# Kernel optimization log

Hardware: AMD Instinct MI355X
Metric: run time of the kernel (lower is better)

The kernel has to match this reference:

```python
import jax, jax.numpy as jnp
import numpy as np

B, T, C, NH = 8, 1024, 768, 12

def setup_inputs() -> dict:
    key = jax.random.key(0)
    k1, k2, k3 = jax.random.split(key, 3)
    x = jax.random.normal(k1, (B, T, C), dtype=jnp.float32)
    Wqkv = jax.random.normal(k2, (C, 3 * C), dtype=jnp.float32) * 0.02
    bqkv = jnp.zeros((3 * C,), dtype=jnp.float32)
    Wproj = jax.random.normal(k3, (C, C), dtype=jnp.float32) * 0.02
    bproj = jnp.zeros((C,), dtype=jnp.float32)
    return {"x": x, "Wqkv": Wqkv, "bqkv": bqkv, "Wproj": Wproj, "bproj": bproj}

def reference(x, Wqkv, bqkv, Wproj, bproj):
    b, t, c = x.shape
    hs = c // NH
    qkv = x @ Wqkv + bqkv  # [B,T,3C]
    q, k, v = jnp.split(qkv, 3, axis=2)
    # [B,T,C] -> [B,NH,T,hs]
    q = q.reshape(b, t, NH, hs).transpose(0, 2, 1, 3)
    k = k.reshape(b, t, NH, hs).transpose(0, 2, 1, 3)
    v = v.reshape(b, t, NH, hs).transpose(0, 2, 1, 3)
    att = jnp.einsum('bhqd,bhkd->bhqk', q, k) * (hs ** -0.5)
    causal = jnp.tril(jnp.ones((t, t), dtype=bool))
    att = jnp.where(causal[None, None], att, jnp.finfo(att.dtype).min)
    att = jax.nn.softmax(att, axis=-1)
    y = jnp.einsum('bhqk,bhkd->bhqd', att, v)
    y = y.transpose(0, 2, 1, 3).reshape(b, t, c)
    return y @ Wproj + bproj
```

## Files before the change

### kernel.cpp

```cpp
#include <hip/hip_runtime.h>

constexpr int Bb  = 8;
constexpr int Tt  = 1024;
constexpr int Cc  = 768;
constexpr int NHh = 12;
constexpr int HS  = 64;
constexpr int C3  = 3 * Cc;

typedef short bf16x8 __attribute__((ext_vector_type(8)));
typedef float f32x4  __attribute__((ext_vector_type(4)));

__device__ inline short bf16r(float f) {
    unsigned u = __float_as_uint(f);
    u += 0x7FFF + ((u >> 16) & 1);
    return (short)(u >> 16);
}
__device__ inline short bf16h(float f) {
    return (short)((__float_as_uint(f) + 0x8000u) >> 16);
}

__global__ __launch_bounds__(256)
void f32_to_bf16(const float* __restrict__ in, short* __restrict__ out, int n) {
    int i = (blockIdx.x * 256 + threadIdx.x) * 4;
    if (i < n) {
        float4 v = *(const float4*)(in + i);
        short4 o;
        o.x = bf16r(v.x); o.y = bf16r(v.y); o.z = bf16r(v.z); o.w = bf16r(v.w);
        *(short4*)(out + i) = o;
    }
}

__global__ __launch_bounds__(1024)
void transpose_to_bf16(const float* __restrict__ in, short* __restrict__ out,
                       int R, int C) {
    __shared__ short tile[32][33];
    int c = blockIdx.x * 32 + threadIdx.x;
    int r = blockIdx.y * 32 + threadIdx.y;
    tile[threadIdx.y][threadIdx.x] = bf16r(in[(size_t)r * C + c]);
    __syncthreads();
    int oc   = blockIdx.y * 32 + threadIdx.x;
    int orow = blockIdx.x * 32 + threadIdx.y;
    out[(size_t)orow * R + oc] = tile[threadIdx.x][threadIdx.y];
}

__global__ __launch_bounds__(256)
void transpose_v(const short* __restrict__ qkv, short* __restrict__ vt) {
    __shared__ short tile[64][65];
    const int bh = blockIdx.y;
    const int b = bh / NHh, h = bh % NHh;
    const int t0 = blockIdx.x * 64;
    const int tx = threadIdx.x & 63, ty = threadIdx.x >> 6;
    const short* src = qkv + ((size_t)b * Tt + t0) * C3 + 2 * Cc + h * HS;
#pragma unroll
    for (int r = 0; r < 16; ++r)
        tile[ty * 16 + r][tx] = src[(size_t)(ty * 16 + r) * C3 + tx];
    __syncthreads();
    short* dst = vt + (size_t)bh * HS * Tt + t0;
#pragma unroll
    for (int r = 0; r < 16; ++r)
        dst[(size_t)(ty * 16 + r) * Tt + tx] = tile[tx][ty * 16 + r];
}

template <int MI, int OB>
__global__ __launch_bounds__(256)
void gemm_mfma_bias(const short* __restrict__ A, const short* __restrict__ Bt,
                    const float* __restrict__ bias, void* __restrict__ Cout,
                    int M, int N, int K) {
    constexpr int TM = MI * 32;
    __shared__ short Als[TM * 64];
    __shared__ short Bls[128 * 64];

    const int t = threadIdx.x, w = t >> 6, lane = t & 63;
    const int m0 = blockIdx.y * TM, n0 = blockIdx.x * 128;

    const int sr = t >> 3;
    const int sg = ((t & 7) ^ (sr & 7)) * 8;

    const short* Ag[MI];
#pragma unroll
    for (int q = 0; q < MI; ++q)
        Ag[q] = A + (size_t)(m0 + q * 32 + sr) * K + sg;
    const short* Bg[4];
#pragma unroll
    for (int q = 0; q < 4; ++q)
        Bg[q] = Bt + (size_t)(n0 + q * 32 + sr) * K + sg;

    char* AlsB = (char*)Als + w * 1024;
    char* BlsB = (char*)Bls + w * 1024;

    const int wm = (w >> 1) * (MI * 16), wn = (w & 1) * 64;
    const int laneM = lane & 15, laneG = lane >> 4;

    f32x4 acc[MI][4] = {};

    for (int kt = 0; kt < K; kt += 64) {
        __syncthreads();
#pragma unroll
        for (int q = 0; q < MI; ++q)
            __builtin_amdgcn_global_load_lds(
                (const __attribute__((address_space(1))) void*)(Ag[q] + kt),
                (__attribute__((address_space(3))) void*)(AlsB + q * 4096), 16, 0, 0);
#pragma unroll
        for (int q = 0; q < 4; ++q)
            __builtin_amdgcn_global_load_lds(
                (const __attribute__((address_space(1))) void*)(Bg[q] + kt),
                (__attribute__((address_space(3))) void*)(BlsB + q * 4096), 16, 0, 0);
        __syncthreads();

#pragma unroll
        for (int ks = 0; ks < 2; ++ks) {
            const int kx = (((ks << 2) + laneG) ^ (laneM & 7)) * 8;
            bf16x8 af[MI], bfr[4];
#pragma unroll
            for (int i = 0; i < MI; ++i)
                af[i] = *(const bf16x8*)&Als[(wm + i * 16 + laneM) * 64 + kx];
#pragma unroll
            for (int j = 0; j < 4; ++j)
                bfr[j] = *(const bf16x8*)&Bls[(wn + j * 16 + laneM) * 64 + kx];
#pragma unroll
            for (int i = 0; i < MI; ++i)
#pragma unroll
                for (int j = 0; j < 4; ++j)
                    acc[i][j] = __builtin_amdgcn_mfma_f32_16x16x32_bf16(
                        af[i], bfr[j], acc[i][j], 0, 0, 0);
        }
    }

    const int rowBase = m0 + wm + laneG * 4;
    const int colBase = n0 + wn + laneM;
#pragma unroll
    for (int j = 0; j < 4; ++j) {
        const int col = colBase + j * 16;
        const float bv = bias[col];
#pragma unroll
        for (int i = 0; i < MI; ++i) {
#pragma unroll
            for (int r = 0; r < 4; ++r) {
                const int row = rowBase + i * 16 + r;
                const float v = acc[i][j][r] + bv;
                if (OB) ((short*)Cout)[(size_t)row * N + col] = bf16r(v);
                else    ((float*)Cout)[(size_t)row * N + col] = v;
            }
        }
    }
}

__global__ __launch_bounds__(256)
void flash_attn(const short* __restrict__ qkv, const short* __restrict__ vt,
                short* __restrict__ y) {
    const int bh = blockIdx.x % (Bb * NHh);
    const int pi = blockIdx.x / (Bb * NHh);
    const int h  = bh % NHh, b = bh / NHh;
    const int t = threadIdx.x, w = t >> 6, lane = t & 63;
    const int laneM = lane & 15, laneG = lane >> 4;

    __shared__ short Kls[64 * 64];
    __shared__ short Vls[64 * 64];
    __shared__ short Pls[4][16 * 72];

    const size_t bT = (size_t)b * Tt;

    bf16x8 onesb;
#pragma unroll
    for (int j = 0; j < 8; ++j) onesb[j] = (short)0x3F80;

    const int srow = t >> 3;
    const int gpos = t & 7;
    char* KlsB = (char*)Kls + w * 1024;
    char* VlsB = (char*)Vls + w * 1024;
    const int gs0 = (gpos ^ (srow & 7)) * 8;

    const short* Kbase = qkv + (bT + srow) * C3 + Cc + h * HS + gs0;
    const short* Vbase = vt + ((size_t)bh * HS + srow) * Tt + gs0;

    constexpr float cexp = 0.18033688f;
    constexpr float moff = -5.7707801f;

#pragma unroll 1
    for (int sub = 0; sub < 2; ++sub) {
        const int qt = sub ? (15 - pi) : pi;
        const int q0 = qt * 64;

        const short* qp = qkv + (bT + q0 + w * 16 + laneM) * C3 + h * HS;
        const bf16x8 qf0 = *(const bf16x8*)(qp + laneG * 8);
        const bf16x8 qf1 = *(const bf16x8*)(qp + 32 + laneG * 8);

        f32x4 oacc[4] = {};
        f32x4 lacc   = {};

        const short* Kg = Kbase;
        const short* Vg = Vbase;
#pragma unroll 1
        for (int kt = 0; kt <= qt; ++kt, Kg += 64 * C3, Vg += 64) {
            __syncthreads();
            __builtin_amdgcn_global_load_lds(
                (const __attribute__((address_space(1))) void*)Kg,
                (__attribute__((address_space(3))) void*)(KlsB), 16, 0, 0);
            __builtin_amdgcn_global_load_lds(
                (const __attribute__((address_space(1))) void*)(Kg + 32 * C3),
                (__attribute__((address_space(3))) void*)(KlsB + 4096), 16, 0, 0);
            __builtin_amdgcn_global_load_lds(
                (const __attribute__((address_space(1))) void*)Vg,
                (__attribute__((address_space(3))) void*)(VlsB), 16, 0, 0);
            __builtin_amdgcn_global_load_lds(
                (const __attribute__((address_space(1))) void*)(Vg + 32 * Tt),
                (__attribute__((address_space(3))) void*)(VlsB + 4096), 16, 0, 0);
            __syncthreads();

            f32x4 sacc[4] = {};
#pragma unroll
            for (int ks = 0; ks < 2; ++ks) {
                const bf16x8 qf = ks ? qf1 : qf0;
#pragma unroll
                for (int nb = 0; nb < 4; ++nb) {
                    const int key = nb * 16 + laneM;
                    const bf16x8 kf = *(const bf16x8*)
                        &Kls[key * 64 + (((ks << 2) + laneG) ^ (key & 7)) * 8];
                    sacc[nb] = __builtin_amdgcn_mfma_f32_16x16x32_bf16(
                        qf, kf, sacc[nb], 0, 0, 0);
                }
            }

            if (kt == qt) {
#pragma unroll
                for (int nb = 0; nb < 4; ++nb) {
                    const int col = nb * 16 + laneM;
#pragma unroll
                    for (int r = 0; r < 4; ++r) {
                        const int row = w * 16 + laneG * 4 + r;
                        if (col > row) sacc[nb][r] = -1e30f;
                    }
                }
            }

            short* Pw = &Pls[w][0];
#pragma unroll
            for (int r = 0; r < 4; ++r)
#pragma unroll
                for (int nb = 0; nb < 4; ++nb) {
                    const float pv = exp2f(fmaf(sacc[nb][r], cexp, moff));
                    Pw[(laneG * 4 + r) * 72 + nb * 16 + laneM] = bf16h(pv);
                }

#pragma unroll
            for (int ks = 0; ks < 2; ++ks) {
                const bf16x8 pf = *(const bf16x8*)&Pw[laneM * 72 + ks * 32 + laneG * 8];
                lacc = __builtin_amdgcn_mfma_f32_16x16x32_bf16(pf, onesb, lacc, 0, 0, 0);
#pragma unroll
                for (int nb = 0; nb < 4; ++nb) {
                    const int d = nb * 16 + laneM;
                    const bf16x8 vf = *(const bf16x8*)
                        &Vls[d * 64 + (((ks << 2) + laneG) ^ (d & 7)) * 8];
                    oacc[nb] = __builtin_amdgcn_mfma_f32_16x16x32_bf16(
                        pf, vf, oacc[nb], 0, 0, 0);
                }
            }
        }

        short* yp = y + (bT + q0 + w * 16) * Cc + h * HS;
#pragma unroll
        for (int r = 0; r < 4; ++r) {
            const float inv = 1.f / lacc[r];
#pragma unroll
            for (int nb = 0; nb < 4; ++nb)
                yp[(size_t)(laneG * 4 + r) * Cc + nb * 16 + laneM] = bf16r(oacc[nb][r] * inv);
        }
    }
}

extern "C" void kernel_launch(void* const* d_in, const int* in_sizes, int n_in,
                              void* d_out, int out_size, void* d_ws, size_t ws_size,
                              hipStream_t stream) {
    const float* x     = (const float*)d_in[0];
    const float* Wqkv  = (const float*)d_in[1];
    const float* bqkv  = (const float*)d_in[2];
    const float* Wproj = (const float*)d_in[3];
    const float* bproj = (const float*)d_in[4];

    constexpr int M = Bb * Tt;
    short* xb     = (short*)d_ws;
    short* wqkvT  = xb     + (size_t)M * Cc;
    short* wprojT = wqkvT  + (size_t)C3 * Cc;
    short* qkv    = wprojT + (size_t)Cc * Cc;
    short* yatt   = qkv    + (size_t)M * C3;
    short* vt     = yatt   + (size_t)M * Cc;

    f32_to_bf16<<<dim3((M * Cc) / 1024), dim3(256), 0, stream>>>(x, xb, M * Cc);
    transpose_to_bf16<<<dim3(C3 / 32, Cc / 32), dim3(32, 32), 0, stream>>>(Wqkv, wqkvT, Cc, C3);
    transpose_to_bf16<<<dim3(Cc / 32, Cc / 32), dim3(32, 32), 0, stream>>>(Wproj, wprojT, Cc, Cc);

    gemm_mfma_bias<4, 1><<<dim3(C3 / 128, M / 128), dim3(256), 0, stream>>>(
        xb, wqkvT, bqkv, qkv, M, C3, Cc);

    transpose_v<<<dim3(Tt / 64, Bb * NHh), dim3(256), 0, stream>>>(qkv, vt);

    flash_attn<<<dim3(Bb * NHh * 8), dim3(256), 0, stream>>>(qkv, vt, yatt);

    gemm_mfma_bias<2, 0><<<dim3(Cc / 128, M / 64), dim3(256), 0, stream>>>(
        yatt, wprojT, bproj, (float*)d_out, M, Cc, Cc);
}
```

Baseline: 199.2 us.

## Double-buffer GEMM LDS tiles with K-step 32 and prefetch next tile

Restructures the bf16 MFMA GEMM main loop to use two LDS buffers of K-width 32 instead of one buffer of width 64. The next K-slice is issued via global_load_lds into the alternate buffer right after the current fragments are read, which leaves one barrier per iteration instead of two. The goal is to overlap global-to-LDS traffic with MFMA work. The trade-offs are twice as many loop iterations, each with half the MFMA work per barrier, and a new swizzle pattern that could raise LDS bank conflicts. The new layout also requires MI to be even.

```diff
diff --git a/kernel.cpp b/kernel.cpp
--- a/kernel.cpp
+++ b/kernel.cpp
@@ -67,63 +67,78 @@
                     const float* __restrict__ bias, void* __restrict__ Cout,
                     int M, int N, int K) {
     constexpr int TM = MI * 32;
-    __shared__ short Als[TM * 64];
-    __shared__ short Bls[128 * 64];
+    __shared__ __align__(16) short Als[2][TM * 32];
+    __shared__ __align__(16) short Bls[2][128 * 32];
 
     const int t = threadIdx.x, w = t >> 6, lane = t & 63;
     const int m0 = blockIdx.y * TM, n0 = blockIdx.x * 128;
 
-    const int sr = t >> 3;
-    const int sg = ((t & 7) ^ (sr & 7)) * 8;
-
-    const short* Ag[MI];
-#pragma unroll
-    for (int q = 0; q < MI; ++q)
-        Ag[q] = A + (size_t)(m0 + q * 32 + sr) * K + sg;
-    const short* Bg[4];
-#pragma unroll
-    for (int q = 0; q < 4; ++q)
-        Bg[q] = Bt + (size_t)(n0 + q * 32 + sr) * K + sg;
-
-    char* AlsB = (char*)Als + w * 1024;
-    char* BlsB = (char*)Bls + w * 1024;
+    const int sr = t >> 2;
+    const int lg = ((t & 3) ^ ((t >> 3) & 3)) * 8;
+
+    const short* Ag[MI / 2];
+#pragma unroll
+    for (int q = 0; q < MI / 2; ++q)
+        Ag[q] = A + (size_t)(m0 + q * 64 + sr) * K + lg;
+    const short* Bg[2];
+#pragma unroll
+    for (int q = 0; q < 2; ++q)
+        Bg[q] = Bt + (size_t)(n0 + q * 64 + sr) * K + lg;
+
+    const int wq = w * 1024;
 
     const int wm = (w >> 1) * (MI * 16), wn = (w & 1) * 64;
     const int laneM = lane & 15, laneG = lane >> 4;
+    const int kx = (laneG ^ ((laneM >> 1) & 3)) * 8;
 
     f32x4 acc[MI][4] = {};
 
-    for (int kt = 0; kt < K; kt += 64) {
+    const int nk = K / 32;
+
+#pragma unroll
+    for (int q = 0; q < MI / 2; ++q)
+        __builtin_amdgcn_global_load_lds(
+            (const __attribute__((address_space(1))) void*)(Ag[q]),
+            (__attribute__((address_space(3))) void*)((char*)&Als[0][0] + q * 4096 + wq), 16, 0, 0);
+#pragma unroll
+    for (int q = 0; q < 2; ++q)
+        __builtin_amdgcn_global_load_lds(
+            (const __attribute__((address_space(1))) void*)(Bg[q]),
+            (__attribute__((address_space(3))) void*)((char*)&Bls[0][0] + q * 4096 + wq), 16, 0, 0);
+
+    for (int kt = 0; kt < nk; ++kt) {
         __syncthreads();
-#pragma unroll
-        for (int q = 0; q < MI; ++q)
-            __builtin_amdgcn_global_load_lds(
-                (const __attribute__((address_space(1))) void*)(Ag[q] + kt),
-                (__attribute__((address_space(3))) void*)(AlsB + q * 4096), 16, 0, 0);
-#pragma unroll
-        for (int q = 0; q < 4; ++q)
-            __builtin_amdgcn_global_load_lds(
-                (const __attribute__((address_space(1))) void*)(Bg[q] + kt),
-                (__attribute__((address_space(3))) void*)(BlsB + q * 4096), 16, 0, 0);
-        __syncthreads();
-
-#pragma unroll
-        for (int ks = 0; ks < 2; ++ks) {
-            const int kx = (((ks << 2) + laneG) ^ (laneM & 7)) * 8;
-            bf16x8 af[MI], bfr[4];
-#pragma unroll
-            for (int i = 0; i < MI; ++i)
-                af[i] = *(const bf16x8*)&Als[(wm + i * 16 + laneM) * 64 + kx];
+
+        const short* Ab = &Als[kt & 1][0];
+        const short* Bb = &Bls[kt & 1][0];
+        bf16x8 af[MI], bfr[4];
+#pragma unroll
+        for (int i = 0; i < MI; ++i)
+            af[i] = *(const bf16x8*)&Ab[(wm + i * 16 + laneM) * 32 + kx];
+#pragma unroll
+        for (int j = 0; j < 4; ++j)
+            bfr[j] = *(const bf16x8*)&Bb[(wn + j * 16 + laneM) * 32 + kx];
+
+        if (kt + 1 < nk) {
+            const int b = (kt + 1) & 1, ko = (kt + 1) * 32;
+#pragma unroll
+            for (int q = 0; q < MI / 2; ++q)
+                __builtin_amdgcn_global_load_lds(
+                    (const __attribute__((address_space(1))) void*)(Ag[q] + ko),
+                    (__attribute__((address_space(3))) void*)((char*)&Als[b][0] + q * 4096 + wq), 16, 0, 0);
+#pragma unroll
+            for (int q = 0; q < 2; ++q)
+                __builtin_amdgcn_global_load_lds(
+                    (const __attribute__((address_space(1))) void*)(Bg[q] + ko),
+                    (__attribute__((address_space(3))) void*)((char*)&Bls[b][0] + q * 4096 + wq), 16, 0, 0);
+        }
+
+#pragma unroll
+        for (int i = 0; i < MI; ++i)
 #pragma unroll
             for (int j = 0; j < 4; ++j)
-                bfr[j] = *(const bf16x8*)&Bls[(wn + j * 16 + laneM) * 64 + kx];
-#pragma unroll
-            for (int i = 0; i < MI; ++i)
-#pragma unroll
-                for (int j = 0; j < 4; ++j)
-                    acc[i][j] = __builtin_amdgcn_mfma_f32_16x16x32_bf16(
-                        af[i], bfr[j], acc[i][j], 0, 0, 0);
-        }
+                acc[i][j] = __builtin_amdgcn_mfma_f32_16x16x32_bf16(
+                    af[i], bfr[j], acc[i][j], 0, 0, 0);
     }
 
     const int rowBase = m0 + wm + laneG * 4;
```

New measurement: 195.2 us. 1.02x faster.
